# Optimization experiments

Measured on AMD Instinct MI355X. Metric: run time of the kernel, lower is better.

The kernel has to match this reference:

```python
import jax, jax.numpy as jnp
import numpy as np

B, N, DEG = 32, 1024, 8
E = B * N * DEG
NT = B * N
F_IN, HID, EDIM, NR, HD = 64, 128, 16, 16, 4
NEG = 0.2  # leaky_relu negative slope (alpha)
K1 = int(np.ceil(0.8 * N))    # 820 kept nodes per graph after pool1
K2 = int(np.ceil(0.8 * K1))   # 656 kept nodes per graph after pool2


def setup_inputs() -> dict:
    key = jax.random.key(0)
    ks = jax.random.split(key, 20)
    nrm = lambda i, shp, s=0.05: jax.random.normal(ks[i], shp, jnp.float32) * s
    x = jax.random.normal(ks[0], (NT, F_IN), jnp.float32)
    off = (jnp.arange(B) * N)[:, None]
    src = (jax.random.randint(ks[1], (B, N * DEG), 0, N) + off).reshape(-1)
    dst = (jax.random.randint(ks[2], (B, N * DEG), 0, N) + off).reshape(-1)
    edge_index = jnp.stack([src, dst]).astype(jnp.int32)
    edge_attr = jax.random.normal(ks[3], (E, EDIM), jnp.float32)
    action = jax.random.normal(ks[4], (B, NR), jnp.float32)
    return dict(
        x=x, edge_attr=edge_attr, action=action,
        W1l=nrm(5, (F_IN, HD * HID)), b1l=jnp.zeros(HD * HID),
        W1r=nrm(6, (F_IN, HD * HID)), b1r=jnp.zeros(HD * HID),
        W1e=nrm(7, (EDIM, HD * HID)), att1=nrm(8, (HD, HID)), bias1=jnp.zeros(HID),
        W2l=nrm(9, (HID, HD * HID)), b2l=jnp.zeros(HD * HID),
        W2r=nrm(10, (HID, HD * HID)), b2r=jnp.zeros(HD * HID),
        W2e=nrm(11, (EDIM, HD * HID)), att2=nrm(12, (HD, HID)), bias2=jnp.zeros(HID),
        p1=nrm(13, (HID,), 0.1), p2=nrm(14, (HID,), 0.1),
        Wf1=nrm(15, (2 * HID + NR, HID)), bf1=jnp.zeros(HID),
        Wf2=nrm(16, (HID, HID)), bf2=jnp.zeros(HID),
        Wf3=nrm(17, (HID, 1), 0.003), bf3=jnp.zeros(1),
        edge_index=edge_index,
    )


def _gatv2(x, edge_index, edge_attr, edge_mask, Wl, bl, Wr, br, We, att, bias):
    # PyG GATv2Conv, concat=False (mean over heads), eval mode (no dropout).
    src, dst = edge_index[0], edge_index[1]
    n = x.shape[0]
    xl = (x @ Wl + bl).reshape(n, HD, HID)   # source transform (x_j)
    xr = (x @ Wr + br).reshape(n, HD, HID)   # target transform (x_i)
    ef = (edge_attr @ We).reshape(-1, HD, HID)
    m = jax.nn.leaky_relu(xl[src] + xr[dst] + ef, NEG)          # [E,H,C]
    logits = jnp.where(edge_mask[:, None], (m * att).sum(-1), -1e9)  # [E,H]
    mx = jax.ops.segment_max(logits, dst, num_segments=n)
    a = jnp.exp(logits - mx[dst])
    den = jax.ops.segment_sum(a, dst, num_segments=n)
    alpha = (a / (den[dst] + 1e-16)) * edge_mask[:, None]       # softmax per dst, masked edges zeroed
    out = jax.ops.segment_sum(xl[src] * alpha[..., None], dst, num_segments=n)
    return out.mean(axis=1) + bias


def _topk(x, node_mask, p, k):
    # PyG TopKPooling: score = x@p/||p||, gate = tanh(score), keep top-k per graph.
    score = (x @ p) / (jnp.linalg.norm(p) + 1e-16)
    gate = jnp.tanh(score)
    s = jnp.where(node_mask, score, -jnp.inf).reshape(B, N)
    idx = jax.lax.top_k(s, k)[1]                                # [B,k]
    keep = jnp.zeros((B, N), bool).at[jnp.arange(B)[:, None], idx].set(True).reshape(-1)
    return x * gate[:, None], keep


def reference(x, edge_attr, action, W1l, b1l, W1r, b1r, W1e, att1, bias1,
              W2l, b2l, W2r, b2r, W2e, att2, bias2, p1, p2,
              Wf1, bf1, Wf2, bf2, Wf3, bf3, edge_index):
    src, dst = edge_index[0], edge_index[1]
    em0 = jnp.ones((E,), bool)
    h = jax.nn.relu(_gatv2(x, edge_index, edge_attr, em0,
                           W1l, b1l, W1r, b1r, W1e, att1, bias1))
    h, keep1 = _topk(h, jnp.ones((NT,), bool), p1, K1)
    em1 = keep1[src] & keep1[dst]
    h = jax.nn.relu(_gatv2(h, edge_index, edge_attr, em1,
                           W2l, b2l, W2r, b2r, W2e, att2, bias2))
    h, keep2 = _topk(h, keep1, p2, K2)
    hb = h.reshape(B, N, HID)
    mb = keep2.reshape(B, N)[..., None]
    gmx = jnp.where(mb, hb, -jnp.inf).max(axis=1)               # global max pool over kept nodes
    gav = (hb * mb).sum(axis=1) / K2                            # global mean pool (K2 kept per graph)
    z = jnp.concatenate([gmx, gav, action], axis=1)             # [B, 2*HID+NR]
    z = jax.nn.relu(z @ Wf1 + bf1)
    z = jax.nn.relu(z @ Wf2 + bf2)
    return z @ Wf3 + bf3
```

## Files before the change

kernel.cpp:

```cpp
#include <hip/hip_runtime.h>
#include <math.h>

#define NTN 32768
#define NBG 32
#define NN  1024
#define EPG 8192
#define EE  262144
#define FIN 64
#define HIDC 128
#define HD  4
#define HC  512
#define EDIM 16
#define NR  16
#define KP1 820
#define KP2 656
#define NKEPT (KP1 * NBG)
#define NEGS 0.2f
#define NPB 2
#define SHIFT 10.0f

template<int K>
__global__ __launch_bounds__(256) void gemm_node3(const float* __restrict__ A,
                                                  const float* __restrict__ Wl,
                                                  const float* __restrict__ bl,
                                                  const float* __restrict__ Wr,
                                                  const float* __restrict__ br,
                                                  const float* __restrict__ gs,
                                                  const int* __restrict__ ids,
                                                  float* __restrict__ Cl,
                                                  float* __restrict__ Cr) {
    __shared__ float a_s[64][K];
    __shared__ int rid_s[64];
    __shared__ float g_s[64];
    int t = threadIdx.x;
    int rb = blockIdx.x >> 2, cg = blockIdx.x & 3;
    int row0 = rb * 64;
    if (t < 64) {
        int rid = ids ? ids[row0 + t] : (row0 + t);
        rid_s[t] = rid;
        g_s[t] = gs ? tanhf(gs[rid]) : 1.0f;
    }
    __syncthreads();
    for (int i = t; i < 64 * K; i += 256) {
        int r = i / K, k = i % K;
        a_s[r][k] = A[(size_t)rid_s[r] * K + k] * g_s[r];
    }
    __syncthreads();
    int tc = cg * 128 + (t & 63) * 2;
    int rg = (t >> 6) * 16;
    float accl0[16], accl1[16], accr0[16], accr1[16];
    float2 blv = *(const float2*)&bl[tc];
    float2 brv = *(const float2*)&br[tc];
    #pragma unroll
    for (int r = 0; r < 16; r++) { accl0[r] = blv.x; accl1[r] = blv.y; accr0[r] = brv.x; accr1[r] = brv.y; }
    for (int k = 0; k < K; k++) {
        float2 wl = *(const float2*)&Wl[(size_t)k * HC + tc];
        float2 wr = *(const float2*)&Wr[(size_t)k * HC + tc];
        #pragma unroll
        for (int r = 0; r < 16; r++) {
            float a = a_s[rg + r][k];
            accl0[r] += a * wl.x; accl1[r] += a * wl.y;
            accr0[r] += a * wr.x; accr1[r] += a * wr.y;
        }
    }
    for (int r = 0; r < 16; r++) {
        size_t base = (size_t)rid_s[rg + r] * HC + tc;
        *(float2*)&Cl[base] = make_float2(accl0[r], accl1[r]);
        *(float2*)&Cr[base] = make_float2(accr0[r], accr1[r]);
    }
}

__global__ __launch_bounds__(1024) void csr_build(const int* __restrict__ dst,
                                                  const int* __restrict__ src,
                                                  int* __restrict__ off,
                                                  int* __restrict__ esrc,
                                                  int* __restrict__ perm,
                                                  const float* __restrict__ p1,
                                                  const float* __restrict__ p2,
                                                  float* __restrict__ pn) {
    int g = blockIdx.x, t = threadIdx.x;
    __shared__ int degS[NN];
    __shared__ int scanS[NN];
    __shared__ int curS[NN];
    degS[t] = 0;
    __syncthreads();
    int eb = g * EPG;
    #pragma unroll
    for (int i = t; i < EPG; i += 1024) atomicAdd(&degS[dst[eb + i] - g * NN], 1);
    __syncthreads();
    int dg = degS[t];
    scanS[t] = dg;
    for (int o = 1; o < NN; o <<= 1) {
        __syncthreads();
        int v = (t >= o) ? scanS[t - o] : 0;
        __syncthreads();
        scanS[t] += v;
    }
    __syncthreads();
    int excl = scanS[t] - dg;
    off[g * NN + t] = eb + excl;
    curS[t] = excl;
    if (g == NBG - 1 && t == NN - 1) off[NTN] = EE;
    if (g == 0 && t < 64) {
        float a = p1[t] * p1[t] + p1[t + 64] * p1[t + 64];
        float b = p2[t] * p2[t] + p2[t + 64] * p2[t + 64];
        #pragma unroll
        for (int sft = 32; sft; sft >>= 1) { a += __shfl_xor(a, sft, 64); b += __shfl_xor(b, sft, 64); }
        if (t == 0) { pn[0] = 1.f / (sqrtf(a) + 1e-16f); pn[1] = 1.f / (sqrtf(b) + 1e-16f); }
    }
    __syncthreads();
    #pragma unroll
    for (int i = t; i < EPG; i += 1024) {
        int e = eb + i;
        int ld = dst[e] - g * NN;
        int p = eb + atomicAdd(&curS[ld], 1);
        esrc[p] = src[e];
        perm[p] = e;
    }
}

__global__ void ea_permute(const int* __restrict__ perm, const float* __restrict__ ea,
                           float* __restrict__ eaP) {
    int id = blockIdx.x * 256 + threadIdx.x;
    int p = id >> 2, q = id & 3;
    ((float4*)eaP)[p * 4 + q] = ((const float4*)ea)[perm[p] * 4 + q];
}

__global__ void esrc_mask(const int* __restrict__ esrc, const int* __restrict__ keep,
                          int* __restrict__ esrc2) {
    int i = blockIdx.x * 256 + threadIdx.x;
    int sv = esrc[i];
    esrc2[i] = keep[sv] ? sv : -1;
}

template<bool L2>
__global__ __launch_bounds__(256) void gat_dst(
        const float* __restrict__ xl, const float* __restrict__ xr,
        const float* __restrict__ eaP, const float* __restrict__ We,
        const float* __restrict__ att, const float* __restrict__ bias,
        const float* __restrict__ pvec, const float* __restrict__ pnInv,
        const int* __restrict__ esrc, const int* __restrict__ off,
        const int* __restrict__ keep,
        float* __restrict__ out, float* __restrict__ score, int nblk) {
    int bid = blockIdx.x;
    int swz = (bid & 7) * (nblk >> 3) + (bid >> 3);
    int d0 = swz * NPB;
    int t = threadIdx.x;
    int w = t >> 6, lane = t & 63;
    int c = w * HIDC + lane * 2;
    __shared__ float red[NPB][HC];
    __shared__ float red2[NPB][HIDC];
    float we0[EDIM], we1[EDIM];
    #pragma unroll
    for (int k = 0; k < EDIM; k++) {
        we0[k] = We[k * HC + c];
        we1[k] = We[k * HC + c + 1];
    }
    float at0 = att[c], at1 = att[c + 1];

    for (int n = 0; n < NPB; n++) {
        int d = d0 + n;
        float denA = 0.f, aA0 = 0.f, aA1 = 0.f;
        float denB = 0.f, aB0 = 0.f, aB1 = 0.f;
        bool live = !L2 || (keep[d] != 0);
        if (live) {
            float2 xrv = *(const float2*)&xr[((size_t)d << 9) + c];
            int e0 = off[d], e1 = off[d + 1];
            int ei = e0;
            for (; ei + 4 <= e1; ei += 4) {
                int s[4]; float mk[4]; float2 xv[4]; float p[4];
                #pragma unroll
                for (int j = 0; j < 4; j++) {
                    int sv = esrc[ei + j];
                    if (L2) {
                        mk[j] = sv >= 0 ? 1.f : 0.f;
                        s[j] = sv >= 0 ? sv : 0;
                    } else {
                        s[j] = sv;
                    }
                }
                #pragma unroll
                for (int j = 0; j < 4; j++) xv[j] = *(const float2*)&xl[((size_t)s[j] << 9) + c];
                #pragma unroll
                for (int j = 0; j < 4; j++) {
                    const float4* eap = (const float4*)(eaP + ((size_t)(ei + j) << 4));
                    float4 E0 = eap[0], E1 = eap[1], E2 = eap[2], E3 = eap[3];
                    float ev[16] = {E0.x, E0.y, E0.z, E0.w, E1.x, E1.y, E1.z, E1.w,
                                    E2.x, E2.y, E2.z, E2.w, E3.x, E3.y, E3.z, E3.w};
                    float ef0 = 0.f, ef1 = 0.f;
                    #pragma unroll
                    for (int k = 0; k < EDIM; k++) { ef0 += ev[k] * we0[k]; ef1 += ev[k] * we1[k]; }
                    float v0 = xv[j].x + xrv.x + ef0; v0 = v0 > 0.f ? v0 : NEGS * v0;
                    float v1 = xv[j].y + xrv.y + ef1; v1 = v1 > 0.f ? v1 : NEGS * v1;
                    p[j] = v0 * at0 + v1 * at1;
                }
                #pragma unroll
                for (int sft = 32; sft; sft >>= 1) {
                    #pragma unroll
                    for (int j = 0; j < 4; j++) p[j] += __shfl_xor(p[j], sft, 64);
                }
                float w0 = __expf(p[0] - SHIFT);
                float w1 = __expf(p[1] - SHIFT);
                float w2 = __expf(p[2] - SHIFT);
                float w3 = __expf(p[3] - SHIFT);
                if (L2) { w0 *= mk[0]; w1 *= mk[1]; w2 *= mk[2]; w3 *= mk[3]; }
                denA += w0; aA0 += w0 * xv[0].x; aA1 += w0 * xv[0].y;
                denB += w1; aB0 += w1 * xv[1].x; aB1 += w1 * xv[1].y;
                denA += w2; aA0 += w2 * xv[2].x; aA1 += w2 * xv[2].y;
                denB += w3; aB0 += w3 * xv[3].x; aB1 += w3 * xv[3].y;
            }
            for (; ei < e1; ei++) {
                int sv = esrc[ei];
                float mk = 1.f;
                int s = sv;
                if (L2) { mk = sv >= 0 ? 1.f : 0.f; s = sv >= 0 ? sv : 0; }
                const float4* eap = (const float4*)(eaP + ((size_t)ei << 4));
                float4 E0 = eap[0], E1 = eap[1], E2 = eap[2], E3 = eap[3];
                float2 xv = *(const float2*)&xl[((size_t)s << 9) + c];
                float ev[16] = {E0.x, E0.y, E0.z, E0.w, E1.x, E1.y, E1.z, E1.w,
                                E2.x, E2.y, E2.z, E2.w, E3.x, E3.y, E3.z, E3.w};
                float ef0 = 0.f, ef1 = 0.f;
                #pragma unroll
                for (int k = 0; k < EDIM; k++) { ef0 += ev[k] * we0[k]; ef1 += ev[k] * we1[k]; }
                float v0 = xv.x + xrv.x + ef0; v0 = v0 > 0.f ? v0 : NEGS * v0;
                float v1 = xv.y + xrv.y + ef1; v1 = v1 > 0.f ? v1 : NEGS * v1;
                float p = v0 * at0 + v1 * at1;
                #pragma unroll
                for (int sft = 32; sft; sft >>= 1) p += __shfl_xor(p, sft, 64);
                float wt = __expf(p - SHIFT);
                if (L2) wt *= mk;
                denA += wt; aA0 += wt * xv.x; aA1 += wt * xv.y;
            }
        }
        float inv = 1.f / (denA + denB + 1e-16f);
        red[n][c] = (aA0 + aB0) * inv;
        red[n][c + 1] = (aA1 + aB1) * inv;
    }
    __syncthreads();
    {
        int n2 = t >> 7, tc = t & 127;
        float v = (red[n2][tc] + red[n2][tc + 128] + red[n2][tc + 256] + red[n2][tc + 384]) * 0.25f
                  + bias[tc];
        v = fmaxf(v, 0.f);
        out[((size_t)(d0 + n2) << 7) + tc] = v;
        red2[n2][tc] = v * pvec[tc];
    }
    __syncthreads();
    if (t < 128) {
        int n3 = t >> 6, l2 = t & 63;
        float sv = red2[n3][l2] + red2[n3][l2 + 64];
        #pragma unroll
        for (int sft = 32; sft; sft >>= 1) sv += __shfl_xor(sv, sft, 64);
        if (l2 == 0) score[d0 + n3] = sv * pnInv[0];
    }
}

__global__ __launch_bounds__(512) void topk_sel(const float* __restrict__ score,
                                                const int* __restrict__ mask, int k,
                                                int* __restrict__ keep, int* __restrict__ klist) {
    __shared__ float v[NN];
    __shared__ short id[NN];
    int g = blockIdx.x, t = threadIdx.x;
    for (int i = t; i < NN; i += 512) {
        int n = g * NN + i;
        bool mk = mask ? (mask[n] != 0) : true;
        v[i] = mk ? score[n] : -INFINITY;
        id[i] = (short)i;
    }
    __syncthreads();
    for (int kk = 2; kk <= NN; kk <<= 1) {
        for (int j = kk >> 1; j > 0; j >>= 1) {
            #pragma unroll 2
            for (int i = t; i < NN; i += 512) {
                int ixj = i ^ j;
                if (ixj > i) {
                    bool up = ((i & kk) == 0);
                    float a = v[i], b2 = v[ixj];
                    short ia = id[i], ib = id[ixj];
                    bool aFirst = (a > b2) || (a == b2 && ia < ib);
                    if (up ? !aFirst : aFirst) { v[i] = b2; v[ixj] = a; id[i] = ib; id[ixj] = ia; }
                }
            }
            __syncthreads();
        }
    }
    for (int i = t; i < NN; i += 512) {
        int kp = (i < k) ? 1 : 0;
        keep[g * NN + id[i]] = kp;
        if (klist && kp) klist[g * k + i] = g * NN + id[i];
    }
}

__global__ __launch_bounds__(512) void tail(const float* __restrict__ score,
                                            const int* __restrict__ mask,
                                            const float* __restrict__ h,
                                            const float* __restrict__ action,
                                            const float* __restrict__ Wf1, const float* __restrict__ bf1,
                                            const float* __restrict__ Wf2, const float* __restrict__ bf2,
                                            const float* __restrict__ Wf3, const float* __restrict__ bf3,
                                            float* __restrict__ out) {
    int g = blockIdx.x, t = threadIdx.x;
    __shared__ float v[NN];
    __shared__ short id[NN];
    __shared__ float gt_s[NN];
    __shared__ char kp_s[NN];
    __shared__ float smx[4][HIDC], ssm[4][HIDC];
    __shared__ float zs[2 * HIDC + NR], z1[HIDC], z2[HIDC], rr[HIDC];
    for (int i = t; i < NN; i += 512) {
        int n = g * NN + i;
        bool mk = (mask[n] != 0);
        v[i] = mk ? score[n] : -INFINITY;
        id[i] = (short)i;
        kp_s[i] = 0;
        gt_s[i] = 0.f;
    }
    __syncthreads();
    for (int kk = 2; kk <= NN; kk <<= 1) {
        for (int j = kk >> 1; j > 0; j >>= 1) {
            #pragma unroll 2
            for (int i = t; i < NN; i += 512) {
                int ixj = i ^ j;
                if (ixj > i) {
                    bool up = ((i & kk) == 0);
                    float a = v[i], b2 = v[ixj];
                    short ia = id[i], ib = id[ixj];
                    bool aFirst = (a > b2) || (a == b2 && ia < ib);
                    if (up ? !aFirst : aFirst) { v[i] = b2; v[ixj] = a; id[i] = ib; id[ixj] = ia; }
                }
            }
            __syncthreads();
        }
    }
    for (int i = t; i < NN; i += 512) {
        if (i < KP2) {
            int nid = id[i];
            kp_s[nid] = 1;
            gt_s[nid] = tanhf(score[g * NN + nid]);
        }
    }
    __syncthreads();
    int c = t & 127, ch = t >> 7;
    float mx = -INFINITY, sm = 0.f;
    for (int n = ch * 256; n < ch * 256 + 256; n++) {
        if (kp_s[n]) {
            float hv = h[(size_t)(g * NN + n) * HIDC + c] * gt_s[n];
            mx = fmaxf(mx, hv);
            sm += hv;
        }
    }
    smx[ch][c] = mx; ssm[ch][c] = sm;
    __syncthreads();
    if (t < HIDC) {
        mx = fmaxf(fmaxf(smx[0][t], smx[1][t]), fmaxf(smx[2][t], smx[3][t]));
        sm = ssm[0][t] + ssm[1][t] + ssm[2][t] + ssm[3][t];
        zs[t] = mx;
        zs[HIDC + t] = sm / (float)KP2;
        if (t < NR) zs[2 * HIDC + t] = action[g * NR + t];
    }
    __syncthreads();
    if (t < HIDC) {
        float a = bf1[t];
        for (int k = 0; k < 2 * HIDC + NR; k++) a += zs[k] * Wf1[(size_t)k * HIDC + t];
        z1[t] = fmaxf(a, 0.f);
    }
    __syncthreads();
    if (t < HIDC) {
        float a = bf2[t];
        for (int k = 0; k < HIDC; k++) a += z1[k] * Wf2[(size_t)k * HIDC + t];
        z2[t] = fmaxf(a, 0.f);
        rr[t] = z2[t] * Wf3[t];
    }
    __syncthreads();
    for (int s = 64; s; s >>= 1) {
        if (t < s) rr[t] += rr[t + s];
        __syncthreads();
    }
    if (t == 0) out[g] = rr[0] + bf3[0];
}

extern "C" void kernel_launch(void* const* d_in, const int* in_sizes, int n_in,
                              void* d_out, int out_size, void* d_ws, size_t ws_size,
                              hipStream_t stream) {
    const float* x    = (const float*)d_in[0];
    const float* ea   = (const float*)d_in[1];
    const float* act  = (const float*)d_in[2];
    const float* W1l  = (const float*)d_in[3];
    const float* b1l  = (const float*)d_in[4];
    const float* W1r  = (const float*)d_in[5];
    const float* b1r  = (const float*)d_in[6];
    const float* W1e  = (const float*)d_in[7];
    const float* att1 = (const float*)d_in[8];
    const float* bias1= (const float*)d_in[9];
    const float* W2l  = (const float*)d_in[10];
    const float* b2l  = (const float*)d_in[11];
    const float* W2r  = (const float*)d_in[12];
    const float* b2r  = (const float*)d_in[13];
    const float* W2e  = (const float*)d_in[14];
    const float* att2 = (const float*)d_in[15];
    const float* bias2= (const float*)d_in[16];
    const float* p1   = (const float*)d_in[17];
    const float* p2   = (const float*)d_in[18];
    const float* Wf1  = (const float*)d_in[19];
    const float* bf1  = (const float*)d_in[20];
    const float* Wf2  = (const float*)d_in[21];
    const float* bf2  = (const float*)d_in[22];
    const float* Wf3  = (const float*)d_in[23];
    const float* bf3  = (const float*)d_in[24];
    const int*   eix  = (const int*)d_in[25];
    const int* srcA = eix;
    const int* dstA = eix + EE;

    float* ws    = (float*)d_ws;
    float* xl    = ws;
    float* xr    = xl + (size_t)NTN * HC;
    float* h     = xr + (size_t)NTN * HC;
    float* score1= h + (size_t)NTN * HIDC;
    float* score2= score1 + NTN;
    float* pn    = score2 + NTN;
    int* keep1 = (int*)(pn + 2);
    int* klist = keep1 + NTN;
    int* off   = klist + NKEPT;
    int* esrc  = off + NTN + 1;
    int* esrc2 = esrc + EE;
    int* perm  = esrc2 + EE;
    float* eaP = (float*)(perm + EE);

    csr_build<<<NBG, 1024, 0, stream>>>(dstA, srcA, off, esrc, perm, p1, p2, pn);
    ea_permute<<<EE * 4 / 256, 256, 0, stream>>>(perm, ea, eaP);

    gemm_node3<FIN><<<(NTN / 64) * 4, 256, 0, stream>>>(x, W1l, b1l, W1r, b1r, nullptr, nullptr, xl, xr);
    gat_dst<false><<<NTN / NPB, 256, 0, stream>>>(xl, xr, eaP, W1e, att1, bias1, p1, pn, esrc, off, nullptr, h, score1, NTN / NPB);

    topk_sel<<<NBG, 512, 0, stream>>>(score1, nullptr, KP1, keep1, klist);

    esrc_mask<<<EE / 256, 256, 0, stream>>>(esrc, keep1, esrc2);
    gemm_node3<HIDC><<<(NKEPT / 64) * 4, 256, 0, stream>>>(h, W2l, b2l, W2r, b2r, score1, klist, xl, xr);
    gat_dst<true><<<NTN / NPB, 256, 0, stream>>>(xl, xr, eaP, W2e, att2, bias2, p2, pn + 1, esrc2, off, keep1, h, score2, NTN / NPB);

    tail<<<NBG, 512, 0, stream>>>(score2, keep1, h, act,
                                  Wf1, bf1, Wf2, bf2, Wf3, bf3, (float*)d_out);
}
```

Baseline: 541.5 us.

## Fuse edge-attr permute into layer-1 GEMM and edge masking into top-k

Removes two small kernel launches. The edge-attribute permutation now runs as a grid-stride tail of the first node GEMM, and the source-edge masking runs inside topk_sel from a shared keep array. gat_dst also gains a minimum-occupancy hint in its launch bounds. This cuts launch overhead, but the permute copy now adds serial work to the GEMM blocks, topk_sel runs only 32 blocks so the masking loop has little parallelism, and the occupancy hint may force register spills.

Result: no change. 530.9 us (-1.9%).

```diff
diff --git a/kernel.cpp b/kernel.cpp
--- a/kernel.cpp
+++ b/kernel.cpp
@@ -28,7 +28,10 @@
                                                   const float* __restrict__ gs,
                                                   const int* __restrict__ ids,
                                                   float* __restrict__ Cl,
-                                                  float* __restrict__ Cr) {
+                                                  float* __restrict__ Cr,
+                                                  const int* __restrict__ perm,
+                                                  const float* __restrict__ ea,
+                                                  float* __restrict__ eaP) {
     __shared__ float a_s[64][K];
     __shared__ int rid_s[64];
     __shared__ float g_s[64];
@@ -68,6 +71,15 @@
         *(float2*)&Cl[base] = make_float2(accl0[r], accl1[r]);
         *(float2*)&Cr[base] = make_float2(accr0[r], accr1[r]);
     }
+    if (perm) {
+        int ng = gridDim.x * 256;
+        for (int p = blockIdx.x * 256 + t; p < EE; p += ng) {
+            int e = perm[p];
+            const float4* s4 = (const float4*)(ea + (size_t)e * EDIM);
+            float4* d4 = (float4*)(eaP + (size_t)p * EDIM);
+            d4[0] = s4[0]; d4[1] = s4[1]; d4[2] = s4[2]; d4[3] = s4[3];
+        }
+    }
 }
 
 __global__ __launch_bounds__(1024) void csr_build(const int* __restrict__ dst,
@@ -119,22 +131,8 @@
     }
 }
 
-__global__ void ea_permute(const int* __restrict__ perm, const float* __restrict__ ea,
-                           float* __restrict__ eaP) {
-    int id = blockIdx.x * 256 + threadIdx.x;
-    int p = id >> 2, q = id & 3;
-    ((float4*)eaP)[p * 4 + q] = ((const float4*)ea)[perm[p] * 4 + q];
-}
-
-__global__ void esrc_mask(const int* __restrict__ esrc, const int* __restrict__ keep,
-                          int* __restrict__ esrc2) {
-    int i = blockIdx.x * 256 + threadIdx.x;
-    int sv = esrc[i];
-    esrc2[i] = keep[sv] ? sv : -1;
-}
-
 template<bool L2>
-__global__ __launch_bounds__(256) void gat_dst(
+__global__ __launch_bounds__(256, 4) void gat_dst(
         const float* __restrict__ xl, const float* __restrict__ xr,
         const float* __restrict__ eaP, const float* __restrict__ We,
         const float* __restrict__ att, const float* __restrict__ bias,
@@ -257,9 +255,12 @@
 
 __global__ __launch_bounds__(512) void topk_sel(const float* __restrict__ score,
                                                 const int* __restrict__ mask, int k,
-                                                int* __restrict__ keep, int* __restrict__ klist) {
+                                                int* __restrict__ keep, int* __restrict__ klist,
+                                                const int* __restrict__ esrc,
+                                                int* __restrict__ esrc2) {
     __shared__ float v[NN];
     __shared__ short id[NN];
+    __shared__ char kpS[NN];
     int g = blockIdx.x, t = threadIdx.x;
     for (int i = t; i < NN; i += 512) {
         int n = g * NN + i;
@@ -287,7 +288,16 @@
     for (int i = t; i < NN; i += 512) {
         int kp = (i < k) ? 1 : 0;
         keep[g * NN + id[i]] = kp;
+        kpS[id[i]] = (char)kp;
         if (klist && kp) klist[g * k + i] = g * NN + id[i];
+    }
+    __syncthreads();
+    if (esrc2) {
+        int eb = g * EPG;
+        for (int i = t; i < EPG; i += 512) {
+            int sv = esrc[eb + i];
+            esrc2[eb + i] = kpS[sv - g * NN] ? sv : -1;
+        }
     }
 }
 
@@ -426,16 +436,18 @@
     float* eaP = (float*)(perm + EE);
 
     csr_build<<<NBG, 1024, 0, stream>>>(dstA, srcA, off, esrc, perm, p1, p2, pn);
-    ea_permute<<<EE * 4 / 256, 256, 0, stream>>>(perm, ea, eaP);
-
-    gemm_node3<FIN><<<(NTN / 64) * 4, 256, 0, stream>>>(x, W1l, b1l, W1r, b1r, nullptr, nullptr, xl, xr);
-    gat_dst<false><<<NTN / NPB, 256, 0, stream>>>(xl, xr, eaP, W1e, att1, bias1, p1, pn, esrc, off, nullptr, h, score1, NTN / NPB);
-
-    topk_sel<<<NBG, 512, 0, stream>>>(score1, nullptr, KP1, keep1, klist);
-
-    esrc_mask<<<EE / 256, 256, 0, stream>>>(esrc, keep1, esrc2);
-    gemm_node3<HIDC><<<(NKEPT / 64) * 4, 256, 0, stream>>>(h, W2l, b2l, W2r, b2r, score1, klist, xl, xr);
-    gat_dst<true><<<NTN / NPB, 256, 0, stream>>>(xl, xr, eaP, W2e, att2, bias2, p2, pn + 1, esrc2, off, keep1, h, score2, NTN / NPB);
+
+    gemm_node3<FIN><<<(NTN / 64) * 4, 256, 0, stream>>>(x, W1l, b1l, W1r, b1r, nullptr, nullptr,
+                                                        xl, xr, perm, ea, eaP);
+    gat_dst<false><<<NTN / NPB, 256, 0, stream>>>(xl, xr, eaP, W1e, att1, bias1, p1, pn, esrc, off,
+                                                  nullptr, h, score1, NTN / NPB);
+
+    topk_sel<<<NBG, 512, 0, stream>>>(score1, nullptr, KP1, keep1, klist, esrc, esrc2);
+
+    gemm_node3<HIDC><<<(NKEPT / 64) * 4, 256, 0, stream>>>(h, W2l, b2l, W2r, b2r, score1, klist,
+                                                           xl, xr, nullptr, nullptr, nullptr);
+    gat_dst<true><<<NTN / NPB, 256, 0, stream>>>(xl, xr, eaP, W2e, att2, bias2, p2, pn + 1, esrc2, off,
+                                                 keep1, h, score2, NTN / NPB);
 
     tail<<<NBG, 512, 0, stream>>>(score2, keep1, h, act,
                                   Wf1, bf1, Wf2, bf2, Wf3, bf3, (float*)d_out);
```
